# Kernel tuning notes

Hardware: AMD Instinct MI355X
Metric: run time of the kernel (lower is better)

The kernel has to match this reference:

```python
import jax, jax.numpy as jnp
import numpy as np

EPS = 1e-12
K_APPNP = 3
ALPHA = 0.5

def setup_inputs() -> dict:
    key = jax.random.key(0)
    kg, kz, k1, k2, k3 = jax.random.split(key, 5)
    N, out_dim, hid_dim = 10000, 128, 256
    g = jax.random.uniform(kg, (N, N), dtype=jnp.float32)
    z = jax.random.normal(kz, (N, out_dim), dtype=jnp.float32)
    def xavier(k, shape):
        fan_out, fan_in = shape
        lim = float(np.sqrt(6.0 / (fan_in + fan_out)))
        return jax.random.uniform(k, shape, jnp.float32, -lim, lim)
    # torch Linear weight is [out_features, in_features]
    W1 = xavier(k1, (hid_dim, out_dim))    # res1: out_dim -> hid_dim
    W1_ = xavier(k2, (hid_dim, hid_dim))   # res1_: hid -> hid
    W2 = xavier(k3, (out_dim, hid_dim))    # res2: hid -> out_dim
    return {"g": g, "z": z, "W1": W1, "W1_": W1_, "W2": W2}

def _graph_conv(g, x, W, act):
    # dropout is identity in eval mode
    return act((g @ x) @ W.T)

def _appnp(g, H):
    Z = H
    for _ in range(K_APPNP):
        Z = (1.0 - ALPHA) * (g @ Z) + ALPHA * H
    return Z

def reference(g, z, W1, W1_, W2):
    z1 = _graph_conv(g, z, W1, jax.nn.relu)       # [N, hid]
    z_ = _graph_conv(g, z1, W1_, jax.nn.relu)     # [N, hid]
    # torch.tensor(z_) detaches from the autograd graph
    zn = jax.lax.stop_gradient(z_)
    norm = jnp.maximum(jnp.linalg.norm(zn, axis=1, keepdims=True), EPS)
    zn = zn / norm                                 # F.normalize(p=2, dim=1)
    Z = _appnp(g, zn)                              # [N, hid]
    res = _graph_conv(g, z_, W2, jax.nn.sigmoid)   # [N, out]
    return (res, Z)
```

## Files before the change

### kernel.cpp

```cpp
#include <hip/hip_runtime.h>
#include <stdint.h>

typedef __attribute__((ext_vector_type(8))) short short8;
typedef __attribute__((ext_vector_type(4))) float f32x4;
typedef __attribute__((ext_vector_type(4))) unsigned short us4;

#define MFMA16(a,b,c) __builtin_amdgcn_mfma_f32_16x16x32_bf16((a),(b),(c),0,0,0)

static __device__ __forceinline__ float bf2f(unsigned short u){
  union { float f; unsigned int i; } c; c.i = ((unsigned int)u) << 16; return c.f;
}
static __device__ __forceinline__ unsigned short f2bf(float f){
  union { float f; unsigned int i; } c; c.f = f;
  unsigned int x = c.i;
  unsigned int r = x + 0x7fffu + ((x >> 16) & 1u);
  return (unsigned short)(r >> 16);
}

typedef const __attribute__((address_space(1))) void cg_void;
typedef __attribute__((address_space(3))) void lds_void;
static __device__ __forceinline__ void gl_lds16(const void* g, void* l){
  __builtin_amdgcn_global_load_lds((cg_void*)g, (lds_void*)l, 16, 0, 0);
}

__global__ void k_conv_g(const float* __restrict__ g, unsigned short* __restrict__ o){
  const int CH = 2512;
  const long long total = 10048LL * CH;
  for (long long i = (long long)blockIdx.x*blockDim.x + threadIdx.x; i < total;
       i += (long long)gridDim.x*blockDim.x){
    int r = (int)(i / CH);
    int c4 = (int)(i % CH) * 4;
    us4 v = {0,0,0,0};
    if (r < 10000 && c4 < 10000){
      float4 f = *(const float4*)(g + (long long)r*10000 + c4);
      v.x = f2bf(f.x); v.y = f2bf(f.y); v.z = f2bf(f.z); v.w = f2bf(f.w);
    }
    *(us4*)(o + (long long)r*10048 + c4) = v;
  }
}

__global__ void k_conv(const float* __restrict__ in, unsigned short* __restrict__ o, int n4){
  for (int i = blockIdx.x*blockDim.x + threadIdx.x; i < n4; i += gridDim.x*blockDim.x){
    float4 f = *(const float4*)(in + (long long)i*4);
    us4 v; v.x=f2bf(f.x); v.y=f2bf(f.y); v.z=f2bf(f.z); v.w=f2bf(f.w);
    *(us4*)(o + (long long)i*4) = v;
  }
}

__global__ void k_tconv_z(const float* __restrict__ z, unsigned short* __restrict__ o){
  __shared__ unsigned short t[64][65];
  const int rb = blockIdx.x*64, cb = blockIdx.y*64;
  #pragma unroll
  for (int it = 0; it < 4; ++it){
    int idx = it*256 + threadIdx.x;
    int r = idx >> 4, c4 = (idx & 15) * 4;
    float4 f = {0.f,0.f,0.f,0.f};
    if (rb + r < 10000) f = *(const float4*)(z + (long long)(rb+r)*128 + cb + c4);
    t[c4+0][r] = f2bf(f.x); t[c4+1][r] = f2bf(f.y);
    t[c4+2][r] = f2bf(f.z); t[c4+3][r] = f2bf(f.w);
  }
  __syncthreads();
  #pragma unroll
  for (int it = 0; it < 4; ++it){
    int idx = it*256 + threadIdx.x;
    int ro = idx >> 4, co4 = (idx & 15) * 4;
    us4 v; v.x=t[ro][co4]; v.y=t[ro][co4+1]; v.z=t[ro][co4+2]; v.w=t[ro][co4+3];
    *(us4*)(o + (long long)(cb+ro)*10048 + rb + co4) = v;
  }
}

__global__ void k_t_bf16(const unsigned short* __restrict__ in, unsigned short* __restrict__ o){
  __shared__ unsigned short t[64][65];
  const int rb = blockIdx.x*64, cb = blockIdx.y*64;
  #pragma unroll
  for (int it = 0; it < 4; ++it){
    int idx = it*256 + threadIdx.x;
    int r = idx >> 4, c4 = (idx & 15) * 4;
    us4 v = {0,0,0,0};
    if (rb + r < 10000) v = *(const us4*)(in + (long long)(rb+r)*256 + cb + c4);
    t[c4+0][r]=v.x; t[c4+1][r]=v.y; t[c4+2][r]=v.z; t[c4+3][r]=v.w;
  }
  __syncthreads();
  #pragma unroll
  for (int it = 0; it < 4; ++it){
    int idx = it*256 + threadIdx.x;
    int ro = idx >> 4, co4 = (idx & 15)*4;
    us4 v; v.x=t[ro][co4]; v.y=t[ro][co4+1]; v.z=t[ro][co4+2]; v.w=t[ro][co4+3];
    *(us4*)(o + (long long)(cb+ro)*10048 + rb + co4) = v;
  }
}

__global__ void k_rownorm(const unsigned short* __restrict__ in, unsigned short* __restrict__ o){
  const int w = threadIdx.x >> 6, l = threadIdx.x & 63;
  const int row = blockIdx.x*4 + w;
  us4 v = *(const us4*)(in + (long long)row*256 + l*4);
  float a = bf2f(v.x), b = bf2f(v.y), c = bf2f(v.z), d = bf2f(v.w);
  float ss = a*a + b*b + c*c + d*d;
  #pragma unroll
  for (int off = 32; off; off >>= 1) ss += __shfl_xor(ss, off, 64);
  float s = 1.0f / fmaxf(sqrtf(ss), 1e-12f);
  us4 r; r.x=f2bf(a*s); r.y=f2bf(b*s); r.z=f2bf(c*s); r.w=f2bf(d*s);
  *(us4*)(o + (long long)row*256 + l*4) = r;
}

template<int BN, int NWM, int NWN>
__global__ __launch_bounds__(256)
void k_gemm(const unsigned short* __restrict__ A,
            const unsigned short* __restrict__ B,
            float* __restrict__ P, int S, int ldp)
{
  constexpr int LDA = 10048;
  constexpr int BM  = 64;
  constexpr int WM = BM / NWM, WN = BN / NWN;
  constexpr int MF = WM / 16, NF = WN / 16;
  constexpr int AE = BM * 64;
  constexpr int BE = BN * 64;
  constexpr int ACH = BM * 8 / 256;
  constexpr int BCH = BN * 8 / 256;

  __shared__ unsigned short sm[2][AE + BE];

  const int tid = threadIdx.x, w = tid >> 6, l = tid & 63;
  const int lr = l & 15, lk = l >> 4, swz = l & 7;
  const int wm = w / NWN, wn = w % NWN;
  const int mBase = blockIdx.x * BM;
  const int nBase = blockIdx.y * BN;
  const int s = blockIdx.z;
  const int kt0 = (157 * s) / S, kt1 = (157 * (s + 1)) / S;

  auto stage = [&](int buf, int kt){
    unsigned short* dst = &sm[buf][0];
    const unsigned short* Ak = A + (long long)kt * 64;
    const unsigned short* Bk = B + (long long)kt * 64;
    #pragma unroll
    for (int i = 0; i < ACH; ++i){
      int c = i * 256 + tid;
      int row = c >> 3, gr = c & 7;
      gl_lds16(Ak + (long long)(mBase + row) * LDA + ((gr ^ (row & 7)) * 8),
               dst + c * 8);
    }
    #pragma unroll
    for (int i = 0; i < BCH; ++i){
      int c = i * 256 + tid;
      int row = c >> 3, gr = c & 7;
      gl_lds16(Bk + (long long)(nBase + row) * LDA + ((gr ^ (row & 7)) * 8),
               dst + AE + c * 8);
    }
  };

  f32x4 acc[MF][NF];
  #pragma unroll
  for (int i = 0; i < MF; ++i)
    #pragma unroll
    for (int j = 0; j < NF; ++j){ f32x4 zz = {0.f,0.f,0.f,0.f}; acc[i][j] = zz; }

  stage(0, kt0);
  int cur = 0;
  for (int kt = kt0; kt < kt1; ++kt){
    __syncthreads();
    if (kt + 1 < kt1) stage(cur ^ 1, kt + 1);
    const unsigned short* sp = &sm[cur][0];
    #pragma unroll
    for (int ks = 0; ks < 2; ++ks){
      short8 a[MF], b[NF];
      #pragma unroll
      for (int i = 0; i < MF; ++i){
        int row = wm * WM + i * 16 + lr;
        a[i] = *(const short8*)(sp + row * 64 + (((4*ks + lk) ^ swz) * 8));
      }
      #pragma unroll
      for (int j = 0; j < NF; ++j){
        int row = wn * WN + j * 16 + lr;
        b[j] = *(const short8*)(sp + AE + row * 64 + (((4*ks + lk) ^ swz) * 8));
      }
      #pragma unroll
      for (int i = 0; i < MF; ++i)
        #pragma unroll
        for (int j = 0; j < NF; ++j)
          acc[i][j] = MFMA16(a[i], b[j], acc[i][j]);
    }
    cur ^= 1;
  }

  float* Pp = P + (long long)s * 10048 * ldp;
  #pragma unroll
  for (int i = 0; i < MF; ++i){
    const int row0 = mBase + wm * WM + i * 16 + lk * 4;
    #pragma unroll
    for (int j = 0; j < NF; ++j){
      const int col = nBase + wn * WN + j * 16 + lr;
      #pragma unroll
      for (int r = 0; r < 4; ++r)
        Pp[(long long)(row0 + r) * ldp + col] = acc[i][j][r];
    }
  }
}

template<int EPI>
__global__ void k_reduce(const float* __restrict__ P, int S, int ldp, int colOff,
                         int lg, void* __restrict__ out, int ldc,
                         const unsigned short* __restrict__ H)
{
  const long long stride = 10048LL * ldp;
  const int idx = blockIdx.x * 256 + threadIdx.x;
  const int row = idx >> lg;
  const int c4 = (idx & ((1 << lg) - 1)) * 4;
  const float* p = P + (long long)row * ldp + colOff + c4;
  float4 sv = *(const float4*)p;
  for (int s2 = 1; s2 < S; ++s2){
    float4 t = *(const float4*)(p + (long long)s2 * stride);
    sv.x += t.x; sv.y += t.y; sv.z += t.z; sv.w += t.w;
  }
  if constexpr (EPI >= 1){
    us4 h = *(const us4*)(H + (long long)row * 256 + c4);
    sv.x = 0.5f*sv.x + 0.5f*bf2f(h.x);
    sv.y = 0.5f*sv.y + 0.5f*bf2f(h.y);
    sv.z = 0.5f*sv.z + 0.5f*bf2f(h.z);
    sv.w = 0.5f*sv.w + 0.5f*bf2f(h.w);
  }
  if constexpr (EPI == 2){
    *(float4*)((float*)out + (long long)row * ldc + c4) = sv;
  } else {
    us4 o; o.x=f2bf(sv.x); o.y=f2bf(sv.y); o.z=f2bf(sv.z); o.w=f2bf(sv.w);
    *(us4*)((unsigned short*)out + (long long)row * ldc + c4) = o;
  }
}

template<int NW, int KW, int ACT>
__global__ __launch_bounds__(320)
void k_gemm_small(const unsigned short* __restrict__ A,
                  const unsigned short* __restrict__ W,
                  void* __restrict__ out)
{
  const int tid = threadIdx.x, w = tid >> 6, l = tid & 63;
  const int lr = l & 15, lk = l >> 4;
  const int mBase = blockIdx.x * 80;
  constexpr int NF = NW/16;

  f32x4 acc[NF];
  #pragma unroll
  for (int f = 0; f < NF; ++f){ f32x4 zz = {0.f,0.f,0.f,0.f}; acc[f] = zz; }

  const unsigned short* ap = A + (long long)(mBase + 16*w + lr)*KW + lk*8;
  #pragma unroll
  for (int kc = 0; kc < KW/32; ++kc){
    short8 a = *(const short8*)(ap + kc*32);
    #pragma unroll
    for (int f = 0; f < NF; ++f){
      short8 b = *(const short8*)(W + (long long)(16*f + lr)*KW + kc*32 + lk*8);
      acc[f] = MFMA16(a, b, acc[f]);
    }
  }

  const int row0 = mBase + 16*w + lk*4;
  #pragma unroll
  for (int f = 0; f < NF; ++f){
    const int col = 16*f + lr;
    #pragma unroll
    for (int r = 0; r < 4; ++r){
      const long long idx = (long long)(row0 + r)*NW + col;
      float v = acc[f][r];
      if constexpr (ACT == 0) ((unsigned short*)out)[idx] = f2bf(fmaxf(v, 0.0f));
      else                    ((float*)out)[idx] = 1.0f / (1.0f + expf(-v));
    }
  }
}

extern "C" void kernel_launch(void* const* d_in, const int* in_sizes, int n_in,
                              void* d_out, int out_size, void* d_ws, size_t ws_size,
                              hipStream_t stream)
{
  const float* g   = (const float*)d_in[0];
  const float* z   = (const float*)d_in[1];
  const float* W1  = (const float*)d_in[2];
  const float* W1_ = (const float*)d_in[3];
  const float* W2  = (const float*)d_in[4];

  char* ws = (char*)d_ws;
  size_t off = 0;
  auto alloc = [&](size_t bytes)->void*{
    void* p = ws + off; off += (bytes + 255) & ~(size_t)255; return p;
  };
  unsigned short* g16  = (unsigned short*)alloc(10048ULL*10048*2);
  unsigned short* zT   = (unsigned short*)alloc(128ULL*10048*2);
  unsigned short* W1c  = (unsigned short*)alloc(256ULL*128*2);
  unsigned short* W1_c = (unsigned short*)alloc(256ULL*256*2);
  unsigned short* W2c  = (unsigned short*)alloc(128ULL*256*2);
  unsigned short* tbuf = (unsigned short*)alloc(10000ULL*256*2);
  unsigned short* Xbuf = (unsigned short*)alloc(10000ULL*256*2);
  unsigned short* Tbuf = (unsigned short*)alloc(512ULL*10048*2);
  unsigned short* zn   = (unsigned short*)alloc(10000ULL*256*2);
  float*          P    = (float*)alloc(10048ULL*1024*4);
  (void)ws_size; (void)in_sizes; (void)n_in; (void)out_size;

  float* res  = (float*)d_out;
  float* Zout = (float*)d_out + 10000LL*128;

  k_conv_g<<<dim3(2048), dim3(256), 0, stream>>>(g, g16);
  k_tconv_z<<<dim3(157,2), dim3(256), 0, stream>>>(z, zT);
  k_conv<<<dim3(32), dim3(256), 0, stream>>>(W1,  W1c,  256*128/4);
  k_conv<<<dim3(64), dim3(256), 0, stream>>>(W1_, W1_c, 256*256/4);
  k_conv<<<dim3(32), dim3(256), 0, stream>>>(W2,  W2c,  128*256/4);

  k_gemm<128,2,2><<<dim3(157,1,3), dim3(256), 0, stream>>>(g16, zT, P, 3, 128);
  k_reduce<0><<<dim3(1250), dim3(256), 0, stream>>>(P, 3, 128, 0, 5, tbuf, 128, nullptr);
  k_gemm_small<256,128,0><<<dim3(125), dim3(320), 0, stream>>>(tbuf, W1c, Xbuf);
  k_t_bf16<<<dim3(157,4), dim3(256), 0, stream>>>(Xbuf, Tbuf);
  k_gemm<256,1,4><<<dim3(157,1,3), dim3(256), 0, stream>>>(g16, Tbuf, P, 3, 256);
  k_reduce<0><<<dim3(2500), dim3(256), 0, stream>>>(P, 3, 256, 0, 6, tbuf, 256, nullptr);
  k_gemm_small<256,256,0><<<dim3(125), dim3(320), 0, stream>>>(tbuf, W1_c, Xbuf);
  k_rownorm<<<dim3(2500), dim3(256), 0, stream>>>(Xbuf, zn);
  k_t_bf16<<<dim3(157,4), dim3(256), 0, stream>>>(Xbuf, Tbuf);
  k_t_bf16<<<dim3(157,4), dim3(256), 0, stream>>>(zn, Tbuf + 256LL*10048);
  k_gemm<256,1,4><<<dim3(157,2,2), dim3(256), 0, stream>>>(g16, Tbuf, P, 2, 512);
  k_reduce<0><<<dim3(2500), dim3(256), 0, stream>>>(P, 2, 512, 0,   6, tbuf, 256, nullptr);
  k_reduce<1><<<dim3(2500), dim3(256), 0, stream>>>(P, 2, 512, 256, 6, Xbuf, 256, zn);
  k_gemm_small<128,256,1><<<dim3(125), dim3(320), 0, stream>>>(tbuf, W2c, res);
  k_t_bf16<<<dim3(157,4), dim3(256), 0, stream>>>(Xbuf, Tbuf);
  k_gemm<256,1,4><<<dim3(157,1,3), dim3(256), 0, stream>>>(g16, Tbuf, P, 3, 256);
  k_reduce<1><<<dim3(2500), dim3(256), 0, stream>>>(P, 3, 256, 0, 6, Xbuf, 256, zn);
  k_t_bf16<<<dim3(157,4), dim3(256), 0, stream>>>(Xbuf, Tbuf);
  k_gemm<256,1,4><<<dim3(157,1,3), dim3(256), 0, stream>>>(g16, Tbuf, P, 3, 256);
  k_reduce<2><<<dim3(2500), dim3(256), 0, stream>>>(P, 3, 256, 0, 6, Zout, 256, zn);
}
```

Before: 632.4 us.

## Add 256x256-tile 8-wave GEMM with quarter-step pipelined LDS staging for g products

Adds a new GEMM kernel with 512 threads and 256x256 output tiles. It stages the next K tile in quarter pieces interleaved with MFMA work, raises wave priority around the MFMAs, and uses more split-K slices. The wider N=256 GEMMs switch to it to cut re-reads of the large bf16 adjacency matrix and improve MFMA density. The adjacency buffer is padded to 10240 rows and the partial buffer is enlarged, which adds conversion work and more split-K partials for the reduce kernels to read.

```diff
diff --git a/kernel.cpp b/kernel.cpp
--- a/kernel.cpp
+++ b/kernel.cpp
@@ -23,9 +23,11 @@
   __builtin_amdgcn_global_load_lds((cg_void*)g, (lds_void*)l, 16, 0, 0);
 }
 
+#define MROWS 10240LL
+
 __global__ void k_conv_g(const float* __restrict__ g, unsigned short* __restrict__ o){
   const int CH = 2512;
-  const long long total = 10048LL * CH;
+  const long long total = 10240LL * CH;
   for (long long i = (long long)blockIdx.x*blockDim.x + threadIdx.x; i < total;
        i += (long long)gridDim.x*blockDim.x){
     int r = (int)(i / CH);
@@ -101,6 +103,117 @@
   float s = 1.0f / fmaxf(sqrtf(ss), 1e-12f);
   us4 r; r.x=f2bf(a*s); r.y=f2bf(b*s); r.z=f2bf(c*s); r.w=f2bf(d*s);
   *(us4*)(o + (long long)row*256 + l*4) = r;
+}
+
+__global__ __launch_bounds__(512)
+void k_gemm8(const unsigned short* __restrict__ A,
+             const unsigned short* __restrict__ B,
+             float* __restrict__ P, int S, int ldp)
+{
+  constexpr int LDA = 10048;
+  __shared__ unsigned short sm[2][32768];
+
+  const int tid = threadIdx.x;
+  const int wid = tid >> 6, l = tid & 63;
+  const int wm = wid >> 2, wn = wid & 3;
+  const int lr = l & 15, lk = l >> 4;
+  const int mBase = blockIdx.x * 256;
+  const int nBase = blockIdx.y * 256;
+  const int s = blockIdx.z;
+  const int kt0 = (157 * s) / S, kt1 = (157 * (s + 1)) / S;
+
+  auto stage_half = [&](unsigned short* dst, int kt, int h){
+    const unsigned short* base = (h < 2) ? A : B;
+    const int rowBase = ((h < 2) ? mBase : nBase) + (h & 1) * 128;
+    const int ldsOff = ((h < 2) ? 0 : 16384) + (h & 1) * 8192;
+    #pragma unroll
+    for (int i = 0; i < 2; ++i){
+      int ch = tid + 512 * i;
+      int row = ch >> 3, gc = (ch & 7) ^ (row & 7);
+      gl_lds16(base + (long long)(rowBase + row) * LDA + kt * 64 + gc * 8,
+               dst + ldsOff + ch * 8);
+    }
+  };
+
+  f32x4 acc[8][4];
+  #pragma unroll
+  for (int i = 0; i < 8; ++i)
+    #pragma unroll
+    for (int j = 0; j < 4; ++j){ f32x4 zz = {0.f,0.f,0.f,0.f}; acc[i][j] = zz; }
+
+  {
+    unsigned short* d0 = &sm[0][0];
+    stage_half(d0, kt0, 0); stage_half(d0, kt0, 1);
+    stage_half(d0, kt0, 2); stage_half(d0, kt0, 3);
+  }
+
+  int cur = 0;
+  for (int kt = kt0; kt < kt1; ++kt){
+    const bool pf = (kt + 1 < kt1);
+    unsigned short* nb = &sm[cur ^ 1][0];
+    const unsigned short* sp = &sm[cur][0];
+    #pragma unroll
+    for (int q = 0; q < 4; ++q){
+      const int ih = q >> 1, jh = q & 1;
+      if (q == 0){
+        if (pf) stage_half(nb, kt + 1, 0);
+        __builtin_amdgcn_sched_barrier(0);
+        if (pf) asm volatile("s_waitcnt vmcnt(2)" ::: "memory");
+        else    asm volatile("s_waitcnt vmcnt(0)" ::: "memory");
+        __builtin_amdgcn_sched_barrier(0);
+        __builtin_amdgcn_s_barrier();
+        __builtin_amdgcn_sched_barrier(0);
+      }
+      short8 af[4][2], bf[2][2];
+      #pragma unroll
+      for (int ii = 0; ii < 4; ++ii){
+        const int row = wm*128 + (ih*4 + ii)*16 + lr;
+        #pragma unroll
+        for (int ks = 0; ks < 2; ++ks)
+          af[ii][ks] = *(const short8*)(sp + row*64 + (((ks*4 + lk) ^ (row & 7)) * 8));
+      }
+      #pragma unroll
+      for (int jj = 0; jj < 2; ++jj){
+        const int row = wn*64 + (jh*2 + jj)*16 + lr;
+        #pragma unroll
+        for (int ks = 0; ks < 2; ++ks)
+          bf[jj][ks] = *(const short8*)(sp + 16384 + row*64 + (((ks*4 + lk) ^ (row & 7)) * 8));
+      }
+      if (q != 0){
+        if (pf) stage_half(nb, kt + 1, q);
+        __builtin_amdgcn_sched_barrier(0);
+        __builtin_amdgcn_s_barrier();
+        __builtin_amdgcn_sched_barrier(0);
+      }
+      __builtin_amdgcn_s_setprio(1);
+      #pragma unroll
+      for (int ks = 0; ks < 2; ++ks)
+        #pragma unroll
+        for (int ii = 0; ii < 4; ++ii)
+          #pragma unroll
+          for (int jj = 0; jj < 2; ++jj)
+            acc[ih*4+ii][jh*2+jj] =
+              MFMA16(af[ii][ks], bf[jj][ks], acc[ih*4+ii][jh*2+jj]);
+      __builtin_amdgcn_s_setprio(0);
+      __builtin_amdgcn_sched_barrier(0);
+      __builtin_amdgcn_s_barrier();
+      __builtin_amdgcn_sched_barrier(0);
+    }
+    cur ^= 1;
+  }
+
+  float* Pp = P + (long long)s * MROWS * ldp;
+  #pragma unroll
+  for (int i = 0; i < 8; ++i){
+    const int row0 = mBase + wm*128 + i*16 + lk*4;
+    #pragma unroll
+    for (int j = 0; j < 4; ++j){
+      const int col = nBase + wn*64 + j*16 + lr;
+      #pragma unroll
+      for (int r = 0; r < 4; ++r)
+        Pp[(long long)(row0 + r)*ldp + col] = acc[i][j][r];
+    }
+  }
 }
 
 template<int BN, int NWM, int NWN>
@@ -182,7 +295,7 @@
     cur ^= 1;
   }
 
-  float* Pp = P + (long long)s * 10048 * ldp;
+  float* Pp = P + (long long)s * MROWS * ldp;
   #pragma unroll
   for (int i = 0; i < MF; ++i){
     const int row0 = mBase + wm * WM + i * 16 + lk * 4;
@@ -201,7 +314,7 @@
                          int lg, void* __restrict__ out, int ldc,
                          const unsigned short* __restrict__ H)
 {
-  const long long stride = 10048LL * ldp;
+  const long long stride = MROWS * ldp;
   const int idx = blockIdx.x * 256 + threadIdx.x;
   const int row = idx >> lg;
   const int c4 = (idx & ((1 << lg) - 1)) * 4;
@@ -281,7 +394,7 @@
   auto alloc = [&](size_t bytes)->void*{
     void* p = ws + off; off += (bytes + 255) & ~(size_t)255; return p;
   };
-  unsigned short* g16  = (unsigned short*)alloc(10048ULL*10048*2);
+  unsigned short* g16  = (unsigned short*)alloc(10240ULL*10048*2);
   unsigned short* zT   = (unsigned short*)alloc(128ULL*10048*2);
   unsigned short* W1c  = (unsigned short*)alloc(256ULL*128*2);
   unsigned short* W1_c = (unsigned short*)alloc(256ULL*256*2);
@@ -290,7 +403,7 @@
   unsigned short* Xbuf = (unsigned short*)alloc(10000ULL*256*2);
   unsigned short* Tbuf = (unsigned short*)alloc(512ULL*10048*2);
   unsigned short* zn   = (unsigned short*)alloc(10000ULL*256*2);
-  float*          P    = (float*)alloc(10048ULL*1024*4);
+  float*          P    = (float*)alloc(10240ULL*1536*4);
   (void)ws_size; (void)in_sizes; (void)n_in; (void)out_size;
 
   float* res  = (float*)d_out;
@@ -306,20 +419,20 @@
   k_reduce<0><<<dim3(1250), dim3(256), 0, stream>>>(P, 3, 128, 0, 5, tbuf, 128, nullptr);
   k_gemm_small<256,128,0><<<dim3(125), dim3(320), 0, stream>>>(tbuf, W1c, Xbuf);
   k_t_bf16<<<dim3(157,4), dim3(256), 0, stream>>>(Xbuf, Tbuf);
-  k_gemm<256,1,4><<<dim3(157,1,3), dim3(256), 0, stream>>>(g16, Tbuf, P, 3, 256);
-  k_reduce<0><<<dim3(2500), dim3(256), 0, stream>>>(P, 3, 256, 0, 6, tbuf, 256, nullptr);
+  k_gemm8<<<dim3(40,1,6), dim3(512), 0, stream>>>(g16, Tbuf, P, 6, 256);
+  k_reduce<0><<<dim3(2500), dim3(256), 0, stream>>>(P, 6, 256, 0, 6, tbuf, 256, nullptr);
   k_gemm_small<256,256,0><<<dim3(125), dim3(320), 0, stream>>>(tbuf, W1_c, Xbuf);
   k_rownorm<<<dim3(2500), dim3(256), 0, stream>>>(Xbuf, zn);
   k_t_bf16<<<dim3(157,4), dim3(256), 0, stream>>>(Xbuf, Tbuf);
   k_t_bf16<<<dim3(157,4), dim3(256), 0, stream>>>(zn, Tbuf + 256LL*10048);
-  k_gemm<256,1,4><<<dim3(157,2,2), dim3(256), 0, stream>>>(g16, Tbuf, P, 2, 512);
-  k_reduce<0><<<dim3(2500), dim3(256), 0, stream>>>(P, 2, 512, 0,   6, tbuf, 256, nullptr);
-  k_reduce<1><<<dim3(2500), dim3(256), 0, stream>>>(P, 2, 512, 256, 6, Xbuf, 256, zn);
+  k_gemm8<<<dim3(40,2,3), dim3(512), 0, stream>>>(g16, Tbuf, P, 3, 512);
+  k_reduce<0><<<dim3(2500), dim3(256), 0, stream>>>(P, 3, 512, 0,   6, tbuf, 256, nullptr);
+  k_reduce<1><<<dim3(2500), dim3(256), 0, stream>>>(P, 3, 512, 256, 6, Xbuf, 256, zn);
   k_gemm_small<128,256,1><<<dim3(125), dim3(320), 0, stream>>>(tbuf, W2c, res);
   k_t_bf16<<<dim3(157,4), dim3(256), 0, stream>>>(Xbuf, Tbuf);
-  k_gemm<256,1,4><<<dim3(157,1,3), dim3(256), 0, stream>>>(g16, Tbuf, P, 3, 256);
-  k_reduce<1><<<dim3(2500), dim3(256), 0, stream>>>(P, 3, 256, 0, 6, Xbuf, 256, zn);
+  k_gemm8<<<dim3(40,1,6), dim3(512), 0, stream>>>(g16, Tbuf, P, 6, 256);
+  k_reduce<1><<<dim3(2500), dim3(256), 0, stream>>>(P, 6, 256, 0, 6, Xbuf, 256, zn);
   k_t_bf16<<<dim3(157,4), dim3(256), 0, stream>>>(Xbuf, Tbuf);
-  k_gemm<256,1,4><<<dim3(157,1,3), dim3(256), 0, stream>>>(g16, Tbuf, P, 3, 256);
-  k_reduce<2><<<dim3(2500), dim3(256), 0, stream>>>(P, 3, 256, 0, 6, Zout, 256, zn);
-}
+  k_gemm8<<<dim3(40,1,6), dim3(512), 0, stream>>>(g16, Tbuf, P, 6, 256);
+  k_reduce<2><<<dim3(2500), dim3(256), 0, stream>>>(P, 6, 256, 0, 6, Zout, 256, zn);
+}
```

Result: slower. 648.6 us (+2.6%).
